# Performance work log

Hardware: AMD Instinct MI355X
Metric: run time of the kernel (lower is better)

The kernel has to match this reference:

```python
import jax, jax.numpy as jnp
import numpy as np

K, S, P = 3, 2, 2  # kernel_size, stride, padding (dilation=1)


def _unfold(xp, k, s, oh, ow):
    """Extract k*k strided patches from a padded array.

    xp: (..., Hp, Wp) -> (..., k*k, oh, ow), window-position ordering (kh, kw)
    matching torch.nn.Unfold (channel-major handled by caller).
    """
    return jnp.stack(
        [xp[..., i:i + s * (oh - 1) + 1:s, j:j + s * (ow - 1) + 1:s]
         for i in range(K) for j in range(K)],
        axis=-3,
    )


def setup_inputs() -> dict:
    key = jax.random.key(0)
    x = jax.random.normal(key, (8, 256, 128, 128), dtype=jnp.float32)
    return {"x": x}


def reference(x):
    b, c, h, w = x.shape
    oh = (h - K + 2 * P) // S + 1
    ow = (w - K + 2 * P) // S + 1

    # channel-wise L2 norm, computed BEFORE unfolding (padding contributes 0 either way)
    n = jnp.sqrt(jnp.sum(x * x, axis=1))            # (b, h, w)
    n_pad = jnp.pad(n, ((0, 0), (P, P), (P, P)))
    n_patch = _unfold(n_pad, K, S, oh, ow)          # (b, k*k, oh, ow)
    # weighting_fn = softmax over the k*k window positions (torch dim=1 of unfolded norm)
    wts = jax.nn.softmax(n_patch, axis=1)           # (b, k*k, oh, ow)

    x_pad = jnp.pad(x, ((0, 0), (0, 0), (P, P), (P, P)))
    x_patch = _unfold(x_pad, K, S, oh, ow)          # (b, c, k*k, oh, ow)

    # weighted sum over window positions
    return jnp.sum(wts[:, None] * x_patch, axis=2)  # (b, c, oh, ow)
```

## Files before the change

### kernel.cpp

```cpp
#include <hip/hip_runtime.h>
#include <math.h>

#define BATCH 8
#define CH    256
#define H     128
#define W     128
#define HW    (H * W)
#define OH    65
#define OW    65
#define NPIX  (OH * OW)
#define TPB   512
#define WAVES 8
#define CPW   (CH / WAVES)

__global__ __launch_bounds__(TPB) void fused_kernel(const float* __restrict__ x,
                                                    float* __restrict__ out) {
    const int b    = blockIdx.x & 7;
    const int oh   = blockIdx.x >> 3;
    const int tid  = threadIdx.x;
    const int lane = tid & 63;
    const int wv   = tid >> 6;

    int  rowc[3];
    bool rv[3];
    #pragma unroll
    for (int r = 0; r < 3; ++r) {
        int ih = oh * 2 + r - 2;
        rv[r]   = (unsigned)ih < (unsigned)H;
        rowc[r] = ih < 0 ? 0 : (ih > H - 1 ? H - 1 : ih);
    }

    __shared__ float part[WAVES][3][W];
    __shared__ float nrm[3][W];
    __shared__ float wls[OH][9];

    const float2* xw2 = (const float2*)x + (size_t)(b * CH + wv * CPW) * (HW / 2);
    const int base0 = rowc[0] * (W / 2) + lane;
    const int base1 = rowc[1] * (W / 2) + lane;
    const int base2 = rowc[2] * (W / 2) + lane;

    float2 xv[CPW][3];
    float2 a0 = {0.f, 0.f}, a1 = {0.f, 0.f}, a2 = {0.f, 0.f};
    #pragma unroll
    for (int c = 0; c < CPW; ++c) {
        const size_t cb = (size_t)c * (HW / 2);
        xv[c][0] = xw2[cb + base0];
        xv[c][1] = xw2[cb + base1];
        xv[c][2] = xw2[cb + base2];
    }
    #pragma unroll
    for (int c = 0; c < CPW; ++c) {
        a0.x += xv[c][0].x * xv[c][0].x; a0.y += xv[c][0].y * xv[c][0].y;
        a1.x += xv[c][1].x * xv[c][1].x; a1.y += xv[c][1].y * xv[c][1].y;
        a2.x += xv[c][2].x * xv[c][2].x; a2.y += xv[c][2].y * xv[c][2].y;
    }
    *(float2*)&part[wv][0][2 * lane] = a0;
    *(float2*)&part[wv][1][2 * lane] = a1;
    *(float2*)&part[wv][2][2 * lane] = a2;
    __syncthreads();

    if (tid < 3 * W) {
        int r = tid >> 7, col = tid & (W - 1);
        float s = 0.f;
        #pragma unroll
        for (int w = 0; w < WAVES; ++w) s += part[w][r][col];
        nrm[r][col] = sqrtf(s);
    }
    __syncthreads();

    if (tid < OH) {
        const int ow  = tid;
        const int iw0 = ow * 2 - 2;
        float nv[9];
        bool  val[9];
        float m = 0.0f;
        #pragma unroll
        for (int kh = 0; kh < 3; ++kh) {
            bool vh = rv[kh];
            #pragma unroll
            for (int kw = 0; kw < 3; ++kw) {
                int iw = iw0 + kw;
                int k  = kh * 3 + kw;
                bool v = vh && ((unsigned)iw < (unsigned)W);
                val[k] = v;
                nv[k]  = v ? nrm[kh][iw] : 0.0f;
                m = fmaxf(m, nv[k]);
            }
        }
        float denom = 0.0f, wt[9];
        #pragma unroll
        for (int k = 0; k < 9; ++k) {
            float e = __expf(nv[k] - m);
            denom += e;
            wt[k] = val[k] ? e : 0.0f;
        }
        float inv = 1.0f / denom;
        #pragma unroll
        for (int k = 0; k < 9; ++k) wls[ow][k] = wt[k] * inv;
    }
    __syncthreads();

    const float wA0 = wls[lane][2], wA1 = wls[lane][5], wA2 = wls[lane][8];
    const float wB0 = wls[lane + 1][0], wC0 = wls[lane + 1][1];
    const float wB1 = wls[lane + 1][3], wC1 = wls[lane + 1][4];
    const float wB2 = wls[lane + 1][6], wC2 = wls[lane + 1][7];

    float* ob = out + (size_t)(b * CH + wv * CPW) * NPIX + (size_t)oh * OW;
    #pragma unroll
    for (int c = 0; c < CPW; ++c) {
        const float vx0 = xv[c][0].x, vy0 = xv[c][0].y;
        const float vx1 = xv[c][1].x, vy1 = xv[c][1].y;
        const float vx2 = xv[c][2].x, vy2 = xv[c][2].y;
        float S = wB0 * vx0 + wC0 * vy0
                + wB1 * vx1 + wC1 * vy1
                + wB2 * vx2 + wC2 * vy2;
        float T = wA0 * vx0 + wA1 * vx1 + wA2 * vx2;
        float Sp = __shfl_up(S, 1);
        float res = (lane == 0) ? T : T + Sp;
        ob[(size_t)c * NPIX + lane] = res;
        if (lane == 63) ob[(size_t)c * NPIX + 64] = S;
    }
}

extern "C" void kernel_launch(void* const* d_in, const int* in_sizes, int n_in,
                              void* d_out, int out_size, void* d_ws, size_t ws_size,
                              hipStream_t stream) {
    const float* x = (const float*)d_in[0];
    float* out = (float*)d_out;
    (void)d_ws; (void)ws_size;
    fused_kernel<<<BATCH * OH, TPB, 0, stream>>>(x, out);
}
```

Before: 215.3 us.

## Re-read input rows in second pass instead of holding them in registers

Stops keeping all 32 channels × 3 rows of input in registers across both phases. The norm pass now streams the loads, and the weighted-sum pass re-reads them from global memory, likely hitting L2. Launch bounds now request a minimum occupancy of 6 and the unrolling is reduced. The aim is to cut register pressure and raise occupancy, at the cost of loading the input twice.

After: 232.2 us. 1.08x slower.

```diff
diff --git a/kernel.cpp b/kernel.cpp
--- a/kernel.cpp
+++ b/kernel.cpp
@@ -13,8 +13,8 @@
 #define WAVES 8
 #define CPW   (CH / WAVES)
 
-__global__ __launch_bounds__(TPB) void fused_kernel(const float* __restrict__ x,
-                                                    float* __restrict__ out) {
+__global__ __launch_bounds__(TPB, 6) void fused_kernel(const float* __restrict__ x,
+                                                       float* __restrict__ out) {
     const int b    = blockIdx.x & 7;
     const int oh   = blockIdx.x >> 3;
     const int tid  = threadIdx.x;
@@ -39,20 +39,16 @@
     const int base1 = rowc[1] * (W / 2) + lane;
     const int base2 = rowc[2] * (W / 2) + lane;
 
-    float2 xv[CPW][3];
     float2 a0 = {0.f, 0.f}, a1 = {0.f, 0.f}, a2 = {0.f, 0.f};
-    #pragma unroll
+    #pragma unroll 8
     for (int c = 0; c < CPW; ++c) {
         const size_t cb = (size_t)c * (HW / 2);
-        xv[c][0] = xw2[cb + base0];
-        xv[c][1] = xw2[cb + base1];
-        xv[c][2] = xw2[cb + base2];
-    }
-    #pragma unroll
-    for (int c = 0; c < CPW; ++c) {
-        a0.x += xv[c][0].x * xv[c][0].x; a0.y += xv[c][0].y * xv[c][0].y;
-        a1.x += xv[c][1].x * xv[c][1].x; a1.y += xv[c][1].y * xv[c][1].y;
-        a2.x += xv[c][2].x * xv[c][2].x; a2.y += xv[c][2].y * xv[c][2].y;
+        float2 v0 = xw2[cb + base0];
+        float2 v1 = xw2[cb + base1];
+        float2 v2 = xw2[cb + base2];
+        a0.x += v0.x * v0.x; a0.y += v0.y * v0.y;
+        a1.x += v1.x * v1.x; a1.y += v1.y * v1.y;
+        a2.x += v2.x * v2.x; a2.y += v2.y * v2.y;
     }
     *(float2*)&part[wv][0][2 * lane] = a0;
     *(float2*)&part[wv][1][2 * lane] = a1;
@@ -106,15 +102,16 @@
     const float wB2 = wls[lane + 1][6], wC2 = wls[lane + 1][7];
 
     float* ob = out + (size_t)(b * CH + wv * CPW) * NPIX + (size_t)oh * OW;
-    #pragma unroll
+    #pragma unroll 4
     for (int c = 0; c < CPW; ++c) {
-        const float vx0 = xv[c][0].x, vy0 = xv[c][0].y;
-        const float vx1 = xv[c][1].x, vy1 = xv[c][1].y;
-        const float vx2 = xv[c][2].x, vy2 = xv[c][2].y;
-        float S = wB0 * vx0 + wC0 * vy0
-                + wB1 * vx1 + wC1 * vy1
-                + wB2 * vx2 + wC2 * vy2;
-        float T = wA0 * vx0 + wA1 * vx1 + wA2 * vx2;
+        const size_t cb = (size_t)c * (HW / 2);
+        float2 v0 = xw2[cb + base0];
+        float2 v1 = xw2[cb + base1];
+        float2 v2 = xw2[cb + base2];
+        float S = wB0 * v0.x + wC0 * v0.y
+                + wB1 * v1.x + wC1 * v1.y
+                + wB2 * v2.x + wC2 * v2.y;
+        float T = wA0 * v0.x + wA1 * v1.x + wA2 * v2.x;
         float Sp = __shfl_up(S, 1);
         float res = (lane == 0) ? T : T + Sp;
         ob[(size_t)c * NPIX + lane] = res;
```
